# Kernel optimization log

Hardware: AMD Instinct MI355X
Metric: run time of the kernel (lower is better)

Reference implementation:

```python
import jax, jax.numpy as jnp
import numpy as np

N_NODES = 50000
N_EDGES = 640000
D_IN = 128
D_H = 128


def gcn_conv(x, edge_index_sl, W, b, n_nodes):
    # x: [N, d_in]; edge_index_sl: [2, E+N] (self-loops already appended)
    h = x @ W  # [N, d_out]
    row, col = edge_index_sl[0], edge_index_sl[1]
    deg = jax.ops.segment_sum(jnp.ones(row.shape[0], dtype=x.dtype), col,
                              num_segments=n_nodes)
    dis = jnp.where(deg > 0, jax.lax.rsqrt(jnp.maximum(deg, 1e-12)), 0.0)
    norm = dis[row] * dis[col]  # [E+N]
    msg = h[row] * norm[:, None]  # gather + scale, [E+N, d_out]
    out = jax.ops.segment_sum(msg, col, num_segments=n_nodes)  # scatter-add
    return out + b


def setup_inputs() -> dict:
    key = jax.random.key(0)
    ks = jax.random.split(key, 9)
    x = jax.random.normal(ks[0], (N_NODES, D_IN), dtype=jnp.float32)
    edge_index = jax.random.randint(ks[1], (2, N_EDGES), 0, N_NODES, dtype=jnp.int64)
    s0 = 1.0 / np.sqrt(D_IN)
    s1 = 1.0 / np.sqrt(D_H)
    W0 = jax.random.uniform(ks[2], (D_IN, D_H), jnp.float32, -s0, s0)
    b0 = jnp.zeros((D_H,), jnp.float32)
    W1 = jax.random.uniform(ks[3], (D_H, D_H), jnp.float32, -s1, s1)
    b1 = jnp.zeros((D_H,), jnp.float32)
    W2 = jax.random.uniform(ks[4], (D_H, D_H), jnp.float32, -s1, s1)
    b2 = jnp.zeros((D_H,), jnp.float32)
    return {"x": x, "edge_index": edge_index, "W0": W0, "b0": b0,
            "W1": W1, "b1": b1, "W2": W2, "b2": b2}


def reference(x, edge_index, W0, b0, W1, b1, W2, b2):
    n = x.shape[0]
    # GCNConv adds self-loops: append (i, i) for every node.
    loops = jnp.arange(n, dtype=edge_index.dtype)
    ei = jnp.concatenate([edge_index, jnp.stack([loops, loops])], axis=1)
    h = x
    for W, b in ((W0, b0), (W1, b1), (W2, b2)):
        h = gcn_conv(h, ei, W, b, n)
        h = jax.nn.relu(h)  # dropout is identity in eval mode
    return h
```

## Files before the change

### kernel.cpp

```cpp
#include <hip/hip_runtime.h>
#include <hip/hip_bf16.h>

#define D 128
#define CAP 64
typedef _Float16 f16;
typedef unsigned short u16;
typedef f16 f16x8 __attribute__((ext_vector_type(8)));
typedef f16 f16x4 __attribute__((ext_vector_type(4)));
typedef float f32x4 __attribute__((ext_vector_type(4)));



__global__ void scatter_cvt_kernel(const int* __restrict__ row, const int* __restrict__ col,
                                   int* __restrict__ fill, u16* __restrict__ ssrc, int E,
                                   const float* __restrict__ W0, const float* __restrict__ W1,
                                   const float* __restrict__ W2,
                                   const float* __restrict__ b0, const float* __restrict__ b1,
                                   const float* __restrict__ b2,
                                   f16* __restrict__ WT, float* __restrict__ bperm) {
    const int EB = (E + 255) >> 8;
    const int b = blockIdx.x;
    if (b < EB) {
        int i = b * 256 + threadIdx.x;
        if (i < E) {
            int d = col[i];
            int p = atomicAdd(&fill[d], 1);
            if (p < CAP) ssrc[(size_t)d * CAP + p] = (u16)row[i];
        }
    } else {
        int id = (b - EB) * 256 + threadIdx.x;
        if (id < 49152) {
            int l = id >> 14;
            int e = id & 16383;
            int j = e >> 7;
            int nn = e & 127;
            int k = (l == 0) ? j : ((j >> 3) + 16 * (j & 7));
            const float* W = (l == 0) ? W0 : (l == 1) ? W1 : W2;
            WT[(size_t)l * 16384 + nn * 128 + j] = (f16)W[k * 128 + nn];
        } else if (id < 49536) {
            int j = id - 49152;
            int l = j >> 7;
            int pos = j & 127;
            int c = 16 * (pos & 7) + (pos >> 3);
            const float* bb = (l == 0) ? b0 : (l == 1) ? b1 : b2;
            bperm[l * 128 + pos] = bb[c];
        }
    }
}


__global__ __launch_bounds__(256) void gemm_mfma(const float* __restrict__ Aptr,
                                                 const f16* __restrict__ WT,
                                                 const int* __restrict__ fill,
                                                 f16* __restrict__ H, int n) {
    __shared__ f16 sW[128 * 128];
    const int tid  = threadIdx.x;
    const int w    = tid >> 6, lane = tid & 63;
    const int q    = lane >> 4, c = lane & 15;
    const int row0 = blockIdx.x * 64;

    int arow = row0 + w * 16 + c;
    if (arow >= n) arow = n - 1;

    f16x8 afr[4];
    {
        float4 x0[4], x1[4];
        #pragma unroll
        for (int t = 0; t < 4; ++t) {
            const float* src = Aptr + (size_t)arow * D + (t * 4 + q) * 8;
            x0[t] = *(const float4*)src;
            x1[t] = *(const float4*)(src + 4);
        }
        #pragma unroll
        for (int t = 0; t < 4; ++t) {
            f16x8 h;
            h[0] = (f16)x0[t].x; h[1] = (f16)x0[t].y; h[2] = (f16)x0[t].z; h[3] = (f16)x0[t].w;
            h[4] = (f16)x1[t].x; h[5] = (f16)x1[t].y; h[6] = (f16)x1[t].z; h[7] = (f16)x1[t].w;
            afr[t] = h;
        }
    }

    #pragma unroll
    for (int i = 0; i < 8; ++i) {
        int f = i * 256 + tid;
        int r = f >> 4, b = f & 15;
        int u = (r << 4) | (b ^ (r & 15));
        *(f16x8*)&sW[u * 8] = *(const f16x8*)&WT[(size_t)r * D + b * 8];
    }
    __syncthreads();

    f32x4 acc[8];
    #pragma unroll
    for (int nt = 0; nt < 8; ++nt) acc[nt] = (f32x4)0.f;

    #pragma unroll
    for (int nt = 0; nt < 8; ++nt) {
        const int rn = nt * 16 + c;
        #pragma unroll
        for (int t = 0; t < 4; ++t) {
            f16x8 bfr = *(const f16x8*)&sW[(((rn << 4) | ((t * 4 + q) ^ c))) * 8];
            acc[nt] = __builtin_amdgcn_mfma_f32_16x16x32_f16(afr[t], bfr, acc[nt], 0, 0, 0);
        }
    }

    const int rbase = row0 + w * 16 + q * 4;
    int4 fv4 = *(const int4*)&fill[rbase];
    #pragma unroll
    for (int reg = 0; reg < 4; ++reg) {
        int grow = rbase + reg;
        if (grow < n) {
            int fv = (reg == 0) ? fv4.x : (reg == 1) ? fv4.y : (reg == 2) ? fv4.z : fv4.w;
            float dv = rsqrtf((float)(fv + 1));
            f16x8 hh;
            #pragma unroll
            for (int nt = 0; nt < 8; ++nt) hh[nt] = (f16)(acc[nt][reg] * dv);
            *(f16x8*)&H[(size_t)grow * D + c * 8] = hh;
        } else {
            const f16x8 z = {};
            *(f16x8*)&H[(size_t)grow * D + c * 8] = z;
        }
    }
}


__global__ __launch_bounds__(256) void fused_agg_gemm(const f16* __restrict__ Hin,
                                                      const int* __restrict__ fill,
                                                      const u16* __restrict__ ssrc,
                                                      const float* __restrict__ bperm,
                                                      const f16* __restrict__ WT,
                                                      f16* __restrict__ Hout, int n) {
    __shared__ f16 sW[128 * 128];
    __shared__ f16 sA[4][16 * 128];
    const int tid  = threadIdx.x;
    const int w    = tid >> 6, lane = tid & 63;
    const int q    = lane >> 4, c = lane & 15;
    const int row0 = blockIdx.x * 64;

    #pragma unroll
    for (int i = 0; i < 8; ++i) {
        int f = i * 256 + tid;
        int r = f >> 4, b = f & 15;
        int u = (r << 4) | (b ^ (r & 15));
        *(f16x8*)&sW[u * 8] = *(const f16x8*)&WT[(size_t)r * D + b * 8];
    }
    __syncthreads();

    const int h32 = (lane >> 5) & 1;
    const int l   = lane & 31;
    const int fo  = l * 4;
    const int zr  = n;
    const float4 bb = *(const float4*)&bperm[fo];

    for (int p = 0; p < 8; ++p) {
        int v = row0 + w * 16 + p * 2 + h32;
        int vc = (v < n) ? v : (n - 1);
        const u16* sp = &ssrc[(size_t)vc * CAP];
        int4 sv0 = *(const int4*)sp;
        int4 sv1 = *(const int4*)(sp + 8);
        f16x4 hv = *(const f16x4*)&Hin[(size_t)vc * D + fo];
        const int truedeg = fill[vc];

        int deg = truedeg > CAP ? CAP : truedeg;
        int nb  = (deg + 15) >> 4;
        int nbo = __shfl_xor(nb, 32);
        const int nbmax = nb > nbo ? nb : nbo;

        float a0 = (float)hv[0], a1 = (float)hv[1], a2 = (float)hv[2], a3 = (float)hv[3];

        for (int b = 0; b < nbmax; ++b) {
            const int4 c0 = sv0, c1 = sv1;
            if (b + 1 < nbmax) {
                sv0 = *(const int4*)(sp + (b + 1) * 16);
                sv1 = *(const int4*)(sp + (b + 1) * 16 + 8);
            }
            const int rem = deg - b * 16;
            const int wv[8] = {c0.x, c0.y, c0.z, c0.w, c1.x, c1.y, c1.z, c1.w};
            f16x4 g[16];
            #pragma unroll
            for (int j = 0; j < 16; ++j) {
                int iv = (wv[j >> 1] >> ((j & 1) * 16)) & 0xffff;
                iv = (j < rem) ? iv : zr;
                g[j] = *(const f16x4*)&Hin[(size_t)iv * D + fo];
            }
            #pragma unroll
            for (int j = 0; j < 16; j += 4) {
                a0 += ((float)g[j][0] + (float)g[j+1][0]) + ((float)g[j+2][0] + (float)g[j+3][0]);
                a1 += ((float)g[j][1] + (float)g[j+1][1]) + ((float)g[j+2][1] + (float)g[j+3][1]);
                a2 += ((float)g[j][2] + (float)g[j+1][2]) + ((float)g[j+2][2] + (float)g[j+3][2]);
                a3 += ((float)g[j][3] + (float)g[j+1][3]) + ((float)g[j+2][3] + (float)g[j+3][3]);
            }
        }

        const float dv = rsqrtf((float)(truedeg + 1));
        f16x4 res;
        res[0] = (f16)fmaxf(fmaf(dv, a0, bb.x), 0.f);
        res[1] = (f16)fmaxf(fmaf(dv, a1, bb.y), 0.f);
        res[2] = (f16)fmaxf(fmaf(dv, a2, bb.z), 0.f);
        res[3] = (f16)fmaxf(fmaf(dv, a3, bb.w), 0.f);

        const int rL = p * 2 + h32;
        *(f16x4*)&sA[w][((((rL << 4) | ((l >> 1) ^ (rL & 15)))) << 3) + (l & 1) * 4] = res;
    }

    f16x8 afr[4];
    #pragma unroll
    for (int t = 0; t < 4; ++t)
        afr[t] = *(const f16x8*)&sA[w][(((c << 4) | ((t * 4 + q) ^ (c & 15)))) << 3];

    f32x4 acc[8];
    #pragma unroll
    for (int nt = 0; nt < 8; ++nt) acc[nt] = (f32x4)0.f;

    #pragma unroll
    for (int nt = 0; nt < 8; ++nt) {
        const int rn = nt * 16 + c;
        #pragma unroll
        for (int t = 0; t < 4; ++t) {
            f16x8 bfr = *(const f16x8*)&sW[(((rn << 4) | ((t * 4 + q) ^ c))) * 8];
            acc[nt] = __builtin_amdgcn_mfma_f32_16x16x32_f16(afr[t], bfr, acc[nt], 0, 0, 0);
        }
    }

    const int rbase = row0 + w * 16 + q * 4;
    int4 fv4 = *(const int4*)&fill[rbase];
    #pragma unroll
    for (int reg = 0; reg < 4; ++reg) {
        int grow = rbase + reg;
        if (grow < n) {
            int fv = (reg == 0) ? fv4.x : (reg == 1) ? fv4.y : (reg == 2) ? fv4.z : fv4.w;
            float dv = rsqrtf((float)(fv + 1));
            f16x8 hh;
            #pragma unroll
            for (int nt = 0; nt < 8; ++nt) hh[nt] = (f16)(acc[nt][reg] * dv);
            *(f16x8*)&Hout[(size_t)grow * D + c * 8] = hh;
        } else {
            const f16x8 z = {};
            *(f16x8*)&Hout[(size_t)grow * D + c * 8] = z;
        }
    }
}


__global__ __launch_bounds__(256) void agg_last(const f16* __restrict__ H,
                                                const int* __restrict__ fill,
                                                const u16* __restrict__ ssrc,
                                                const float* __restrict__ bperm,
                                                float* __restrict__ out, int n) {
    const int tid  = threadIdx.x;
    const int wid  = (blockIdx.x << 2) | (tid >> 6);
    const int half = (tid >> 5) & 1;
    const int l    = tid & 31;
    int v = wid * 2 + half;
    const bool valid = (v < n);
    if (!valid) v = n - 1;
    const int fo = l * 4;
    const int zr = n;

    const u16* sp = &ssrc[(size_t)v * CAP];
    int4 sv0 = *(const int4*)sp;
    int4 sv1 = *(const int4*)(sp + 8);
    f16x4 hv = *(const f16x4*)&H[(size_t)v * D + fo];
    const int truedeg = fill[v];

    int deg = truedeg > CAP ? CAP : truedeg;
    int nb  = (deg + 15) >> 4;
    int nbo = __shfl_xor(nb, 32);
    const int nbmax = nb > nbo ? nb : nbo;

    float a0 = (float)hv[0], a1 = (float)hv[1], a2 = (float)hv[2], a3 = (float)hv[3];

    for (int b = 0; b < nbmax; ++b) {
        const int4 c0 = sv0, c1 = sv1;
        if (b + 1 < nbmax) {
            sv0 = *(const int4*)(sp + (b + 1) * 16);
            sv1 = *(const int4*)(sp + (b + 1) * 16 + 8);
        }
        const int rem = deg - b * 16;
        const int wv[8] = {c0.x, c0.y, c0.z, c0.w, c1.x, c1.y, c1.z, c1.w};
        f16x4 g[16];
        #pragma unroll
        for (int j = 0; j < 16; ++j) {
            int iv = (wv[j >> 1] >> ((j & 1) * 16)) & 0xffff;
            iv = (j < rem) ? iv : zr;
            g[j] = *(const f16x4*)&H[(size_t)iv * D + fo];
        }
        #pragma unroll
        for (int j = 0; j < 16; j += 4) {
            a0 += ((float)g[j][0] + (float)g[j+1][0]) + ((float)g[j+2][0] + (float)g[j+3][0]);
            a1 += ((float)g[j][1] + (float)g[j+1][1]) + ((float)g[j+2][1] + (float)g[j+3][1]);
            a2 += ((float)g[j][2] + (float)g[j+1][2]) + ((float)g[j+2][2] + (float)g[j+3][2]);
            a3 += ((float)g[j][3] + (float)g[j+1][3]) + ((float)g[j+2][3] + (float)g[j+3][3]);
        }
    }

    const float dv = rsqrtf((float)(truedeg + 1));
    const float4 bb = *(const float4*)&bperm[fo];
    float r0 = fmaxf(fmaf(dv, a0, bb.x), 0.f);
    float r1 = fmaxf(fmaf(dv, a1, bb.y), 0.f);
    float r2 = fmaxf(fmaf(dv, a2, bb.z), 0.f);
    float r3 = fmaxf(fmaf(dv, a3, bb.w), 0.f);

    if (valid) {
        const int cb = (l & 1) * 64 + (l >> 1);
        float* op = out + (size_t)v * D + cb;
        op[0]  = r0;
        op[16] = r1;
        op[32] = r2;
        op[48] = r3;
    }
}


extern "C" void kernel_launch(void* const* d_in, const int* in_sizes, int n_in,
                              void* d_out, int out_size, void* d_ws, size_t ws_size,
                              hipStream_t stream) {
    const float* x  = (const float*)d_in[0];
    const int*   ei = (const int*)d_in[1];
    const float* W0 = (const float*)d_in[2];
    const float* b0 = (const float*)d_in[3];
    const float* W1 = (const float*)d_in[4];
    const float* b1 = (const float*)d_in[5];
    const float* W2 = (const float*)d_in[6];
    const float* b2 = (const float*)d_in[7];
    float* out = (float*)d_out;

    const int n = in_sizes[0] / D;
    const int E = in_sizes[1] / 2;
    const int n_pad = (n + 64) & ~63;
    const int* row = ei;
    const int* col = ei + E;
    const int EB = (E + 255) / 256;

    char* w = (char*)d_ws;
    size_t o = 0;
    f16* hbufA = (f16*)(w + o); o += (size_t)n_pad * D * 2;
    f16* hbufB = (f16*)(w + o); o += (size_t)n_pad * D * 2;
    f16* WT    = (f16*)(w + o); o += (size_t)3 * 16384 * 2;
    o = (o + 63) & ~(size_t)63;
    float* bperm = (float*)(w + o); o += 3 * 128 * 4;
    int* fill = (int*)(w + o); o += (size_t)n_pad * 4;
    o = (o + 127) & ~(size_t)127;
    u16* ssrc = (u16*)(w + o);

    hipMemsetAsync(fill, 0, (size_t)n_pad * 4, stream);
    scatter_cvt_kernel<<<EB + 194, 256, 0, stream>>>(row, col, fill, ssrc, E,
                                                     W0, W1, W2, b0, b1, b2, WT, bperm);

    const int gblocks = n_pad >> 6;
    const int aggwaves = (n + 1) >> 1;
    const int ablocks = (aggwaves + 3) >> 2;

    gemm_mfma<<<gblocks, 256, 0, stream>>>(x, WT, fill, hbufA, n);
    fused_agg_gemm<<<gblocks, 256, 0, stream>>>(hbufA, fill, ssrc, bperm, WT + 16384,
                                                hbufB, n);
    fused_agg_gemm<<<gblocks, 256, 0, stream>>>(hbufB, fill, ssrc, bperm + 128,
                                                WT + 2 * 16384, hbufA, n);
    agg_last<<<ablocks, 256, 0, stream>>>(hbufA, fill, ssrc, bperm + 256, out, n);
}
```

Baseline: 252.6 us.

## Double waves per block in fused aggregation-GEMM and prefetch next node metadata

The fused aggregate+GEMM kernel moves to 512 threads per block, so each wave aggregates 8 rows instead of 16. It now shares one 64-row sA tile across waves behind a barrier, and each wave computes half the output columns of one 16-row tile in the MFMA stage. The next node's neighbour list, features and degree are prefetched during the current node's first gather batch, and the W tile load is issued after the first node loads. The goal is more memory-level parallelism and shorter serial per-wave chains in the latency-bound gather. The cost is an added block-wide barrier, higher register pressure from launch_bounds(512,6), and narrower f16x4 output stores.

```diff
diff --git a/kernel.cpp b/kernel.cpp
--- a/kernel.cpp
+++ b/kernel.cpp
@@ -123,56 +123,58 @@
 }
 
 
-__global__ __launch_bounds__(256) void fused_agg_gemm(const f16* __restrict__ Hin,
-                                                      const int* __restrict__ fill,
-                                                      const u16* __restrict__ ssrc,
-                                                      const float* __restrict__ bperm,
-                                                      const f16* __restrict__ WT,
-                                                      f16* __restrict__ Hout, int n) {
+__global__ __launch_bounds__(512, 6) void fused_agg_gemm(const f16* __restrict__ Hin,
+                                                         const int* __restrict__ fill,
+                                                         const u16* __restrict__ ssrc,
+                                                         const float* __restrict__ bperm,
+                                                         const f16* __restrict__ WT,
+                                                         f16* __restrict__ Hout, int n) {
     __shared__ f16 sW[128 * 128];
-    __shared__ f16 sA[4][16 * 128];
+    __shared__ f16 sA[64 * 128];
     const int tid  = threadIdx.x;
     const int w    = tid >> 6, lane = tid & 63;
     const int q    = lane >> 4, c = lane & 15;
     const int row0 = blockIdx.x * 64;
 
-    #pragma unroll
-    for (int i = 0; i < 8; ++i) {
-        int f = i * 256 + tid;
-        int r = f >> 4, b = f & 15;
-        int u = (r << 4) | (b ^ (r & 15));
-        *(f16x8*)&sW[u * 8] = *(const f16x8*)&WT[(size_t)r * D + b * 8];
-    }
-    __syncthreads();
-
     const int h32 = (lane >> 5) & 1;
     const int l   = lane & 31;
     const int fo  = l * 4;
     const int zr  = n;
+
+    const int vbase = row0 + w * 8 + h32;
+    int vc = (vbase < n) ? vbase : (n - 1);
+    const u16* sp = &ssrc[(size_t)vc * CAP];
+    int4 sv0 = *(const int4*)sp;
+    int4 sv1 = *(const int4*)(sp + 8);
+    f16x4 hv = *(const f16x4*)&Hin[(size_t)vc * D + fo];
+    int truedeg = fill[vc];
+
+    #pragma unroll
+    for (int i = 0; i < 4; ++i) {
+        int f = i * 512 + tid;
+        int r = f >> 4, b = f & 15;
+        int u = (r << 4) | (b ^ (r & 15));
+        *(f16x8*)&sW[u * 8] = *(const f16x8*)&WT[(size_t)r * D + b * 8];
+    }
+
     const float4 bb = *(const float4*)&bperm[fo];
 
-    for (int p = 0; p < 8; ++p) {
-        int v = row0 + w * 16 + p * 2 + h32;
-        int vc = (v < n) ? v : (n - 1);
-        const u16* sp = &ssrc[(size_t)vc * CAP];
-        int4 sv0 = *(const int4*)sp;
-        int4 sv1 = *(const int4*)(sp + 8);
-        f16x4 hv = *(const f16x4*)&Hin[(size_t)vc * D + fo];
-        const int truedeg = fill[vc];
-
+    #pragma unroll
+    for (int p = 0; p < 4; ++p) {
         int deg = truedeg > CAP ? CAP : truedeg;
         int nb  = (deg + 15) >> 4;
         int nbo = __shfl_xor(nb, 32);
         const int nbmax = nb > nbo ? nb : nbo;
 
         float a0 = (float)hv[0], a1 = (float)hv[1], a2 = (float)hv[2], a3 = (float)hv[3];
+        const int tdeg_cur = truedeg;
+        const u16* sp_cur = sp;
+
+        int4 nsv0, nsv1; f16x4 nhv; int ndeg = 0; const u16* nsp = sp;
 
         for (int b = 0; b < nbmax; ++b) {
-            const int4 c0 = sv0, c1 = sv1;
-            if (b + 1 < nbmax) {
-                sv0 = *(const int4*)(sp + (b + 1) * 16);
-                sv1 = *(const int4*)(sp + (b + 1) * 16 + 8);
-            }
+            const int4 c0 = (b == 0) ? sv0 : *(const int4*)(sp_cur + b * 16);
+            const int4 c1 = (b == 0) ? sv1 : *(const int4*)(sp_cur + b * 16 + 8);
             const int rem = deg - b * 16;
             const int wv[8] = {c0.x, c0.y, c0.z, c0.w, c1.x, c1.y, c1.z, c1.w};
             f16x4 g[16];
@@ -182,6 +184,15 @@
                 iv = (j < rem) ? iv : zr;
                 g[j] = *(const f16x4*)&Hin[(size_t)iv * D + fo];
             }
+            if (b == 0 && p < 3) {
+                int vn = vbase + (p + 1) * 2;
+                int vnc = (vn < n) ? vn : (n - 1);
+                nsp  = &ssrc[(size_t)vnc * CAP];
+                nsv0 = *(const int4*)nsp;
+                nsv1 = *(const int4*)(nsp + 8);
+                nhv  = *(const f16x4*)&Hin[(size_t)vnc * D + fo];
+                ndeg = fill[vnc];
+            }
             #pragma unroll
             for (int j = 0; j < 16; j += 4) {
                 a0 += ((float)g[j][0] + (float)g[j+1][0]) + ((float)g[j+2][0] + (float)g[j+3][0]);
@@ -191,37 +202,43 @@
             }
         }
 
-        const float dv = rsqrtf((float)(truedeg + 1));
+        const float dv = rsqrtf((float)(tdeg_cur + 1));
         f16x4 res;
         res[0] = (f16)fmaxf(fmaf(dv, a0, bb.x), 0.f);
         res[1] = (f16)fmaxf(fmaf(dv, a1, bb.y), 0.f);
         res[2] = (f16)fmaxf(fmaf(dv, a2, bb.z), 0.f);
         res[3] = (f16)fmaxf(fmaf(dv, a3, bb.w), 0.f);
 
-        const int rL = p * 2 + h32;
-        *(f16x4*)&sA[w][((((rL << 4) | ((l >> 1) ^ (rL & 15)))) << 3) + (l & 1) * 4] = res;
-    }
+        const int rL = w * 8 + p * 2 + h32;
+        *(f16x4*)&sA[((((rL << 4) | ((l >> 1) ^ (rL & 15)))) << 3) + (l & 1) * 4] = res;
+
+        sv0 = nsv0; sv1 = nsv1; hv = nhv; truedeg = ndeg; sp = nsp;
+    }
+
+    __syncthreads();
+
+    const int tr = w >> 1, ch = w & 1;
 
     f16x8 afr[4];
     #pragma unroll
     for (int t = 0; t < 4; ++t)
-        afr[t] = *(const f16x8*)&sA[w][(((c << 4) | ((t * 4 + q) ^ (c & 15)))) << 3];
-
-    f32x4 acc[8];
-    #pragma unroll
-    for (int nt = 0; nt < 8; ++nt) acc[nt] = (f32x4)0.f;
-
-    #pragma unroll
-    for (int nt = 0; nt < 8; ++nt) {
-        const int rn = nt * 16 + c;
+        afr[t] = *(const f16x8*)&sA[((((tr * 16 + c) << 4) | ((t * 4 + q) ^ c))) << 3];
+
+    f32x4 acc[4];
+    #pragma unroll
+    for (int j = 0; j < 4; ++j) acc[j] = (f32x4)0.f;
+
+    #pragma unroll
+    for (int j = 0; j < 4; ++j) {
+        const int rn = (ch * 4 + j) * 16 + c;
         #pragma unroll
         for (int t = 0; t < 4; ++t) {
             f16x8 bfr = *(const f16x8*)&sW[(((rn << 4) | ((t * 4 + q) ^ c))) * 8];
-            acc[nt] = __builtin_amdgcn_mfma_f32_16x16x32_f16(afr[t], bfr, acc[nt], 0, 0, 0);
-        }
-    }
-
-    const int rbase = row0 + w * 16 + q * 4;
+            acc[j] = __builtin_amdgcn_mfma_f32_16x16x32_f16(afr[t], bfr, acc[j], 0, 0, 0);
+        }
+    }
+
+    const int rbase = row0 + tr * 16 + q * 4;
     int4 fv4 = *(const int4*)&fill[rbase];
     #pragma unroll
     for (int reg = 0; reg < 4; ++reg) {
@@ -229,13 +246,13 @@
         if (grow < n) {
             int fv = (reg == 0) ? fv4.x : (reg == 1) ? fv4.y : (reg == 2) ? fv4.z : fv4.w;
             float dv = rsqrtf((float)(fv + 1));
-            f16x8 hh;
+            f16x4 hh;
             #pragma unroll
-            for (int nt = 0; nt < 8; ++nt) hh[nt] = (f16)(acc[nt][reg] * dv);
-            *(f16x8*)&Hout[(size_t)grow * D + c * 8] = hh;
+            for (int j = 0; j < 4; ++j) hh[j] = (f16)(acc[j][reg] * dv);
+            *(f16x4*)&Hout[(size_t)grow * D + c * 8 + ch * 4] = hh;
         } else {
-            const f16x8 z = {};
-            *(f16x8*)&Hout[(size_t)grow * D + c * 8] = z;
+            const f16x4 z = {};
+            *(f16x4*)&Hout[(size_t)grow * D + c * 8 + ch * 4] = z;
         }
     }
 }
@@ -351,9 +368,9 @@
     const int ablocks = (aggwaves + 3) >> 2;
 
     gemm_mfma<<<gblocks, 256, 0, stream>>>(x, WT, fill, hbufA, n);
-    fused_agg_gemm<<<gblocks, 256, 0, stream>>>(hbufA, fill, ssrc, bperm, WT + 16384,
+    fused_agg_gemm<<<gblocks, 512, 0, stream>>>(hbufA, fill, ssrc, bperm, WT + 16384,
                                                 hbufB, n);
-    fused_agg_gemm<<<gblocks, 256, 0, stream>>>(hbufB, fill, ssrc, bperm + 128,
+    fused_agg_gemm<<<gblocks, 512, 0, stream>>>(hbufB, fill, ssrc, bperm + 128,
                                                 WT + 2 * 16384, hbufA, n);
     agg_last<<<ablocks, 256, 0, stream>>>(hbufA, fill, ssrc, bperm + 256, out, n);
 }
```

Result: faster. 223.4 us (-11.5%).

## Restructure fused aggregate-GEMM into small 16-row blocks without shared weight staging

Applied to the files above, without the earlier changes.

The fused aggregation+GEMM kernel now uses 512-thread blocks that each own 16 rows. Each wave aggregates two nodes once, with no 8-iteration serial loop, and then computes one 16-column output tile by reading W fragments straight from global/L2 instead of staging all of W in LDS. The aim is higher occupancy and more parallel gather latency hiding, and it drops the 32KB LDS footprint. In exchange, W is read per block from cache, output stores become scalar 2-byte strided writes, and the index-prefetch software pipelining is removed in both aggregation kernels.

```diff
diff --git a/kernel.cpp b/kernel.cpp
--- a/kernel.cpp
+++ b/kernel.cpp
@@ -123,129 +123,111 @@
 }
 
 
-__global__ __launch_bounds__(256) void fused_agg_gemm(const f16* __restrict__ Hin,
-                                                      const int* __restrict__ fill,
-                                                      const u16* __restrict__ ssrc,
-                                                      const float* __restrict__ bperm,
-                                                      const f16* __restrict__ WT,
-                                                      f16* __restrict__ Hout, int n) {
-    __shared__ f16 sW[128 * 128];
-    __shared__ f16 sA[4][16 * 128];
+__global__ __launch_bounds__(512, 8) void fused_agg_gemm(const f16* __restrict__ Hin,
+                                                         const int* __restrict__ fill,
+                                                         const u16* __restrict__ ssrc,
+                                                         const float* __restrict__ bperm,
+                                                         const f16* __restrict__ WT,
+                                                         f16* __restrict__ Hout, int n) {
+    __shared__ f16 sA[16 * 128];
     const int tid  = threadIdx.x;
     const int w    = tid >> 6, lane = tid & 63;
     const int q    = lane >> 4, c = lane & 15;
-    const int row0 = blockIdx.x * 64;
-
-    #pragma unroll
-    for (int i = 0; i < 8; ++i) {
-        int f = i * 256 + tid;
-        int r = f >> 4, b = f & 15;
-        int u = (r << 4) | (b ^ (r & 15));
-        *(f16x8*)&sW[u * 8] = *(const f16x8*)&WT[(size_t)r * D + b * 8];
-    }
-    __syncthreads();
+    const int row0 = blockIdx.x * 16;
 
     const int h32 = (lane >> 5) & 1;
     const int l   = lane & 31;
     const int fo  = l * 4;
     const int zr  = n;
+
+    const int v = row0 + w * 2 + h32;
+    const int vc = (v < n) ? v : (n - 1);
+    const u16* sp = &ssrc[(size_t)vc * CAP];
+    int4 sv0 = *(const int4*)sp;
+    int4 sv1 = *(const int4*)(sp + 8);
+    f16x4 hv = *(const f16x4*)&Hin[(size_t)vc * D + fo];
+    const int truedeg = fill[vc];
     const float4 bb = *(const float4*)&bperm[fo];
 
-    for (int p = 0; p < 8; ++p) {
-        int v = row0 + w * 16 + p * 2 + h32;
-        int vc = (v < n) ? v : (n - 1);
-        const u16* sp = &ssrc[(size_t)vc * CAP];
-        int4 sv0 = *(const int4*)sp;
-        int4 sv1 = *(const int4*)(sp + 8);
-        f16x4 hv = *(const f16x4*)&Hin[(size_t)vc * D + fo];
-        const int truedeg = fill[vc];
-
-        int deg = truedeg > CAP ? CAP : truedeg;
-        int nb  = (deg + 15) >> 4;
-        int nbo = __shfl_xor(nb, 32);
-        const int nbmax = nb > nbo ? nb : nbo;
-
-        float a0 = (float)hv[0], a1 = (float)hv[1], a2 = (float)hv[2], a3 = (float)hv[3];
-
-        for (int b = 0; b < nbmax; ++b) {
-            const int4 c0 = sv0, c1 = sv1;
-            if (b + 1 < nbmax) {
-                sv0 = *(const int4*)(sp + (b + 1) * 16);
-                sv1 = *(const int4*)(sp + (b + 1) * 16 + 8);
-            }
-            const int rem = deg - b * 16;
-            const int wv[8] = {c0.x, c0.y, c0.z, c0.w, c1.x, c1.y, c1.z, c1.w};
-            f16x4 g[16];
-            #pragma unroll
-            for (int j = 0; j < 16; ++j) {
-                int iv = (wv[j >> 1] >> ((j & 1) * 16)) & 0xffff;
-                iv = (j < rem) ? iv : zr;
-                g[j] = *(const f16x4*)&Hin[(size_t)iv * D + fo];
-            }
-            #pragma unroll
-            for (int j = 0; j < 16; j += 4) {
-                a0 += ((float)g[j][0] + (float)g[j+1][0]) + ((float)g[j+2][0] + (float)g[j+3][0]);
-                a1 += ((float)g[j][1] + (float)g[j+1][1]) + ((float)g[j+2][1] + (float)g[j+3][1]);
-                a2 += ((float)g[j][2] + (float)g[j+1][2]) + ((float)g[j+2][2] + (float)g[j+3][2]);
-                a3 += ((float)g[j][3] + (float)g[j+1][3]) + ((float)g[j+2][3] + (float)g[j+3][3]);
-            }
-        }
-
-        const float dv = rsqrtf((float)(truedeg + 1));
-        f16x4 res;
-        res[0] = (f16)fmaxf(fmaf(dv, a0, bb.x), 0.f);
-        res[1] = (f16)fmaxf(fmaf(dv, a1, bb.y), 0.f);
-        res[2] = (f16)fmaxf(fmaf(dv, a2, bb.z), 0.f);
-        res[3] = (f16)fmaxf(fmaf(dv, a3, bb.w), 0.f);
-
-        const int rL = p * 2 + h32;
-        *(f16x4*)&sA[w][((((rL << 4) | ((l >> 1) ^ (rL & 15)))) << 3) + (l & 1) * 4] = res;
-    }
+    int deg = truedeg > CAP ? CAP : truedeg;
+    int nb  = (deg + 15) >> 4;
+    int nbo = __shfl_xor(nb, 32);
+    const int nbmax = nb > nbo ? nb : nbo;
+
+    float a0 = (float)hv[0], a1 = (float)hv[1], a2 = (float)hv[2], a3 = (float)hv[3];
+
+    for (int b = 0; b < nbmax; ++b) {
+        int4 c0, c1;
+        if (b == 0) { c0 = sv0; c1 = sv1; }
+        else {
+            c0 = *(const int4*)(sp + b * 16);
+            c1 = *(const int4*)(sp + b * 16 + 8);
+        }
+        const int rem = deg - b * 16;
+        const int wv[8] = {c0.x, c0.y, c0.z, c0.w, c1.x, c1.y, c1.z, c1.w};
+        f16x4 g[16];
+        #pragma unroll
+        for (int j = 0; j < 16; ++j) {
+            int iv = (wv[j >> 1] >> ((j & 1) * 16)) & 0xffff;
+            iv = (j < rem) ? iv : zr;
+            g[j] = *(const f16x4*)&Hin[(size_t)iv * D + fo];
+        }
+        #pragma unroll
+        for (int j = 0; j < 16; j += 4) {
+            a0 += ((float)g[j][0] + (float)g[j+1][0]) + ((float)g[j+2][0] + (float)g[j+3][0]);
+            a1 += ((float)g[j][1] + (float)g[j+1][1]) + ((float)g[j+2][1] + (float)g[j+3][1]);
+            a2 += ((float)g[j][2] + (float)g[j+1][2]) + ((float)g[j+2][2] + (float)g[j+3][2]);
+            a3 += ((float)g[j][3] + (float)g[j+1][3]) + ((float)g[j+2][3] + (float)g[j+3][3]);
+        }
+    }
+
+    const float dv = rsqrtf((float)(truedeg + 1));
+    f16x4 res;
+    res[0] = (f16)fmaxf(fmaf(dv, a0, bb.x), 0.f);
+    res[1] = (f16)fmaxf(fmaf(dv, a1, bb.y), 0.f);
+    res[2] = (f16)fmaxf(fmaf(dv, a2, bb.z), 0.f);
+    res[3] = (f16)fmaxf(fmaf(dv, a3, bb.w), 0.f);
+
+    const int rL = w * 2 + h32;
+    *(f16x4*)&sA[((((rL << 4) | ((l >> 1) ^ rL))) << 3) + (l & 1) * 4] = res;
+
+    __syncthreads();
 
     f16x8 afr[4];
     #pragma unroll
     for (int t = 0; t < 4; ++t)
-        afr[t] = *(const f16x8*)&sA[w][(((c << 4) | ((t * 4 + q) ^ (c & 15)))) << 3];
-
-    f32x4 acc[8];
-    #pragma unroll
-    for (int nt = 0; nt < 8; ++nt) acc[nt] = (f32x4)0.f;
-
-    #pragma unroll
-    for (int nt = 0; nt < 8; ++nt) {
-        const int rn = nt * 16 + c;
-        #pragma unroll
-        for (int t = 0; t < 4; ++t) {
-            f16x8 bfr = *(const f16x8*)&sW[(((rn << 4) | ((t * 4 + q) ^ c))) * 8];
-            acc[nt] = __builtin_amdgcn_mfma_f32_16x16x32_f16(afr[t], bfr, acc[nt], 0, 0, 0);
-        }
-    }
-
-    const int rbase = row0 + w * 16 + q * 4;
+        afr[t] = *(const f16x8*)&sA[(((c << 4) | ((t * 4 + q) ^ c))) << 3];
+
+    f32x4 acc = (f32x4)0.f;
+    const int rn = w * 16 + c;
+    #pragma unroll
+    for (int t = 0; t < 4; ++t) {
+        f16x8 bfr = *(const f16x8*)&WT[(size_t)rn * D + (t * 4 + q) * 8];
+        acc = __builtin_amdgcn_mfma_f32_16x16x32_f16(afr[t], bfr, acc, 0, 0, 0);
+    }
+
+    const int rbase = row0 + q * 4;
     int4 fv4 = *(const int4*)&fill[rbase];
     #pragma unroll
     for (int reg = 0; reg < 4; ++reg) {
         int grow = rbase + reg;
+        float av = (reg == 0) ? acc[0] : (reg == 1) ? acc[1] : (reg == 2) ? acc[2] : acc[3];
         if (grow < n) {
             int fv = (reg == 0) ? fv4.x : (reg == 1) ? fv4.y : (reg == 2) ? fv4.z : fv4.w;
-            float dv = rsqrtf((float)(fv + 1));
-            f16x8 hh;
-            #pragma unroll
-            for (int nt = 0; nt < 8; ++nt) hh[nt] = (f16)(acc[nt][reg] * dv);
-            *(f16x8*)&Hout[(size_t)grow * D + c * 8] = hh;
+            float dvo = rsqrtf((float)(fv + 1));
+            Hout[(size_t)grow * D + c * 8 + w] = (f16)(av * dvo);
         } else {
-            const f16x8 z = {};
-            *(f16x8*)&Hout[(size_t)grow * D + c * 8] = z;
-        }
-    }
-}
-
-
-__global__ __launch_bounds__(256) void agg_last(const f16* __restrict__ H,
-                                                const int* __restrict__ fill,
-                                                const u16* __restrict__ ssrc,
-                                                const float* __restrict__ bperm,
-                                                float* __restrict__ out, int n) {
+            Hout[(size_t)grow * D + c * 8 + w] = (f16)0.f;
+        }
+    }
+}
+
+
+__global__ __launch_bounds__(256, 8) void agg_last(const f16* __restrict__ H,
+                                                   const int* __restrict__ fill,
+                                                   const u16* __restrict__ ssrc,
+                                                   const float* __restrict__ bperm,
+                                                   float* __restrict__ out, int n) {
     const int tid  = threadIdx.x;
     const int wid  = (blockIdx.x << 2) | (tid >> 6);
     const int half = (tid >> 5) & 1;
@@ -270,10 +252,11 @@
     float a0 = (float)hv[0], a1 = (float)hv[1], a2 = (float)hv[2], a3 = (float)hv[3];
 
     for (int b = 0; b < nbmax; ++b) {
-        const int4 c0 = sv0, c1 = sv1;
-        if (b + 1 < nbmax) {
-            sv0 = *(const int4*)(sp + (b + 1) * 16);
-            sv1 = *(const int4*)(sp + (b + 1) * 16 + 8);
+        int4 c0, c1;
+        if (b == 0) { c0 = sv0; c1 = sv1; }
+        else {
+            c0 = *(const int4*)(sp + b * 16);
+            c1 = *(const int4*)(sp + b * 16 + 8);
         }
         const int rem = deg - b * 16;
         const int wv[8] = {c0.x, c0.y, c0.z, c0.w, c1.x, c1.y, c1.z, c1.w};
@@ -347,13 +330,14 @@
                                                      W0, W1, W2, b0, b1, b2, WT, bperm);
 
     const int gblocks = n_pad >> 6;
+    const int fblocks = n_pad >> 4;
     const int aggwaves = (n + 1) >> 1;
     const int ablocks = (aggwaves + 3) >> 2;
 
     gemm_mfma<<<gblocks, 256, 0, stream>>>(x, WT, fill, hbufA, n);
-    fused_agg_gemm<<<gblocks, 256, 0, stream>>>(hbufA, fill, ssrc, bperm, WT + 16384,
+    fused_agg_gemm<<<fblocks, 512, 0, stream>>>(hbufA, fill, ssrc, bperm, WT + 16384,
                                                 hbufB, n);
-    fused_agg_gemm<<<gblocks, 256, 0, stream>>>(hbufB, fill, ssrc, bperm + 128,
+    fused_agg_gemm<<<fblocks, 512, 0, stream>>>(hbufB, fill, ssrc, bperm + 128,
                                                 WT + 2 * 16384, hbufA, n);
     agg_last<<<ablocks, 256, 0, stream>>>(hbufA, fill, ssrc, bperm + 256, out, n);
 }
```

Result: faster. 236.7 us (-6.3%).
